# Optimization experiments

Hardware: AMD Instinct MI355X
Metric: run time of the kernel (lower is better)

Reference implementation:

```python
import jax, jax.numpy as jnp
import numpy as np
from jax import lax

DN = ('NCHW', 'OIHW', 'NCHW')

def conv3x3(x, w, b):
    y = lax.conv_general_dilated(x, w, (1, 1), 'SAME', dimension_numbers=DN)
    return y + b[None, :, None, None]

def box_filter(x, ws):
    # depthwise WxW averaging conv, VALID after reflect pad
    C = x.shape[1]
    k = jnp.ones((C, 1, ws, ws), x.dtype) / (ws * ws)
    return lax.conv_general_dilated(x, k, (1, 1), 'VALID', feature_group_count=C,
                                    dimension_numbers=DN)

def compute_std_map(features, ws):
    N, C, H, W = features.shape
    pad = ws // 2
    fp = jnp.pad(features, ((0, 0), (0, 0), (pad, pad), (pad, pad)), mode='reflect')
    local_mean = box_filter(fp, ws)            # [N,C,H,W]
    local_mean_sq = box_filter(fp * fp, ws)
    local_var = jnp.clip(local_mean_sq - local_mean ** 2, 1e-6, None)
    if C == 4:
        cw = jax.nn.softmax(jnp.array([1.0, 1.5, 1.0, 1.5], features.dtype))
    else:
        cw = jax.nn.softmax(jnp.ones((C,), features.dtype))
    result = jnp.sum(jnp.sqrt(local_var) * cw[None, :, None, None], axis=1, keepdims=True)
    return result ** 0.8                        # [N,1,H,W]

def setup_inputs() -> dict:
    key = jax.random.key(0)
    ks = jax.random.split(key, 10)
    inp = {}
    inp['x'] = jax.random.normal(ks[0], (1, 4, 1024, 1024), jnp.float32)
    inp['w1'] = jax.random.normal(ks[1], (32, 4, 3, 3), jnp.float32) * (1.0 / np.sqrt(4 * 9))
    inp['b1'] = jax.random.normal(ks[2], (32,), jnp.float32) * 0.01
    inp['w2'] = jax.random.normal(ks[3], (16, 32, 3, 3), jnp.float32) * (1.0 / np.sqrt(32 * 9))
    inp['b2'] = jax.random.normal(ks[4], (16,), jnp.float32) * 0.01
    inp['w3'] = jax.random.normal(ks[5], (8, 16, 3, 3), jnp.float32) * (1.0 / np.sqrt(16 * 9))
    inp['b3'] = jax.random.normal(ks[6], (8,), jnp.float32) * 0.01
    inp['channel_weights'] = jnp.ones((4,), jnp.float32) / 4.0
    inp['fusion_w'] = jnp.full((1, 3, 1, 1), 1.0 / 3.0, jnp.float32) + \
        jax.random.normal(ks[7], (1, 3, 1, 1), jnp.float32) * 0.02
    inp['fusion_b'] = jnp.zeros((1,), jnp.float32)
    return inp

def reference(x, w1, b1, w2, b2, w3, b3, channel_weights, fusion_w, fusion_b):
    window_sizes = [11, 25, 49]
    # feature extractor
    f = jax.nn.leaky_relu(conv3x3(x, w1, b1), 0.2)
    f = jax.nn.leaky_relu(conv3x3(f, w2, b2), 0.2)
    f = conv3x3(f, w3, b3)                      # [B,8,H,W]
    # multi-scale std maps
    maps = jnp.concatenate([compute_std_map(f, ws) for ws in window_sizes], axis=1)  # [B,3,H,W]
    fused = jax.nn.relu(
        lax.conv_general_dilated(maps, fusion_w, (1, 1), 'VALID', dimension_numbers=DN)
        + fusion_b[None, :, None, None])        # [B,1,H,W]
    # adaptive thresholds
    std_flat = fused.reshape(-1)
    q25 = jnp.quantile(std_flat, 0.25)
    q75 = jnp.quantile(std_flat, 0.75)
    iqr75 = q75 - q25
    global_std = jnp.std(x, axis=(2, 3), keepdims=True, ddof=1)   # [B,4,1,1]
    lower = (q25 - 0.5 * iqr75) * jnp.ones_like(global_std)
    upper = (q75 + 0.5 * iqr75) * jnp.ones_like(global_std)
    gf = jnp.clip(global_std * 5.0, 0.5, 2.0)
    lower = lower * gf
    upper = upper * gf
    cwn = jax.nn.softmax(channel_weights).reshape(1, 4, 1, 1)
    channel_std = jnp.std(x * cwn, axis=(2, 3), keepdims=True, ddof=1)
    cf = jnp.clip(channel_std * 2.0, 0.8, 1.2)
    lower = lower * cf
    upper = upper * cf
    # texture mask
    q30 = jnp.quantile(std_flat, 0.3)
    q70 = jnp.quantile(std_flat, 0.7)
    lower_mean = jnp.mean(lower, axis=1, keepdims=True)           # [B,1,1,1]
    upper_mean = jnp.mean(upper, axis=1, keepdims=True)
    l_t = 0.5 * lower_mean + 0.5 * q30
    u_t = 0.5 * upper_mean + 0.5 * q70
    iqr = q70 - q30
    widen = iqr < 0.01
    l_t = jnp.where(widen, l_t - iqr, l_t)
    u_t = jnp.where(widen, u_t + iqr, u_t)
    diff = u_t - l_t
    mid0 = (l_t + u_t) / 2
    narrow = diff < 0.02
    l_t = jnp.where(narrow, mid0 - 0.01, l_t)
    u_t = jnp.where(narrow, mid0 + 0.01, u_t)
    midpoint = (l_t + u_t) / 2
    scale = u_t - l_t
    normalized = jax.nn.sigmoid(4.0 * (fused - midpoint) / scale)
    nm = jnp.mean(normalized)
    mask = jnp.where(nm > 0.65, 0.1 + 0.5 * normalized,
                     jnp.where(nm < 0.35, 0.2 + 0.5 * normalized,
                               0.15 + 0.55 * normalized))
    return mask
```

## Files before the change

### kernel.cpp

```cpp
#include <hip/hip_runtime.h>
#include <stdint.h>

constexpr int H = 1024, W = 1024;
constexpr int NPIX = H * W;
constexpr int PADM = 24;
constexpr int PROW = W + 2 * PADM;

constexpr size_t OFF_F1H   = 0;
constexpr size_t OFF_F1L   = 67108864;
constexpr size_t OFF_F2H   = 134217728;
constexpr size_t OFF_F2L   = 167772160;
constexpr size_t OFF_F3    = 0;
constexpr size_t OFF_HF    = 33554432;
constexpr size_t OFF_HF2   = 67108864;
constexpr size_t OFF_MAPS  = 100663296;
constexpr size_t OFF_FUSED = OFF_MAPS + 3UL * 4194304;
constexpr size_t OFF_NORM  = OFF_FUSED + 4194304;
constexpr size_t OFF_SMALL = 201326592;
constexpr size_t OFF_STATS  = OFF_SMALL;
constexpr size_t OFF_NMSUM  = OFF_SMALL + 64;
constexpr size_t OFF_HIST   = OFF_SMALL + 128;
constexpr size_t OFF_RSTATE = OFF_HIST + 8192;
constexpr size_t OFF_SCAL   = OFF_RSTATE + 64;
constexpr size_t OFF_WT     = OFF_SCAL + 64;

using short8  = __attribute__((ext_vector_type(8))) short;
using short4v = __attribute__((ext_vector_type(4))) short;
using f32x4   = __attribute__((ext_vector_type(4))) float;

__device__ __forceinline__ int reflect1024(int j) {
    return j < 0 ? -j : (j > 1023 ? 2046 - j : j);
}
__device__ __forceinline__ unsigned short rne_bf16(float v) {
    uint32_t u = __float_as_uint(v);
    return (unsigned short)((u + 0x7FFFu + ((u >> 16) & 1u)) >> 16);
}
__device__ __forceinline__ float bf16f(unsigned short h) {
    return __uint_as_float(((uint32_t)h) << 16);
}

__global__ void wfrag_kernel(const float* __restrict__ w, unsigned short* __restrict__ wfH,
                             unsigned short* __restrict__ wfL, int CIN, int COUT, int NF, int S) {
    int total = NF * S * 512;
    int e = blockIdx.x * 256 + threadIdx.x;
    if (e >= total) return;
    int j = e & 7, l = (e >> 3) & 63;
    int rest = e >> 9;
    int s = rest % S, nf = rest / S;
    int k = s * 32 + ((l >> 4) << 3) + j;
    int n = (l & 15) + 16 * nf;
    float v = 0.f;
    if (k < 9 * CIN && n < COUT) {
        int kk = k / CIN, c = k % CIN;
        int ky = kk / 3, kx = kk - ky * 3;
        v = w[((n * CIN + c) * 3 + ky) * 3 + kx];
    }
    unsigned short h = rne_bf16(v);
    wfH[e] = h;
    wfL[e] = rne_bf16(v - bf16f(h));
}

template <int CIN, int COUT, int S, bool LEAKY, int OUT_MODE, int IN_MODE, int MINW>
__global__ __launch_bounds__(256, MINW) void mconv_kernel(
        const void* __restrict__ inA, const void* __restrict__ inB,
        const unsigned short* __restrict__ wfH, const unsigned short* __restrict__ wfL,
        const float* __restrict__ bias, void* __restrict__ outA, void* __restrict__ outB) {
    constexpr int NF = (COUT + 15) / 16;
    constexpr int RS = 66 * CIN;
    __shared__ __align__(16) unsigned short Ah[6 * RS];
    __shared__ __align__(16) unsigned short Al[6 * RS];

    const int tid = threadIdx.x;
    const int bx = blockIdx.x * 64, by = blockIdx.y * 4;
    const int lane = tid & 63, rw = tid >> 6;

    if constexpr (IN_MODE == 1) {
        constexpr int CROW = RS / 8;
        constexpr int LCP  = (CIN == 32) ? 2 : 1;
        constexpr int TOT  = 12 * CROW;
        constexpr int NLOAD = (TOT + 255) / 256;
        const unsigned short* gh = (const unsigned short*)inA;
        const unsigned short* gl = (const unsigned short*)inB;

        short8 regs[NLOAD];
#pragma unroll
        for (int k = 0; k < NLOAD; ++k) {
            int idx = tid + k * 256;
            short8 v = short8{0, 0, 0, 0, 0, 0, 0, 0};
            if (idx < TOT) {
                int ar = idx / CROW;
                int j  = idx - ar * CROW;
                int r  = ar >> 1;
                int a  = ar & 1;
                int gy = by - 1 + r;
                int gx = bx - 1 + (j >> LCP);
                if ((unsigned)gy < 1024u && (unsigned)gx < 1024u) {
                    const unsigned short* g = (a ? gl : gh) +
                        ((size_t)gy << 10) * CIN + (size_t)(bx - 1) * CIN + (size_t)j * 8;
                    v = *(const short8*)g;
                }
            }
            regs[k] = v;
        }
#pragma unroll
        for (int k = 0; k < NLOAD; ++k) {
            int idx = tid + k * 256;
            if (idx < TOT) {
                int ar = idx / CROW;
                int j  = idx - ar * CROW;
                int r  = ar >> 1;
                int a  = ar & 1;
                unsigned short* dst = (a ? Al : Ah) + r * RS + j * 8;
                *(short8*)dst = regs[k];
            }
        }
    } else {
        constexpr int TOT = 6 * 4 * 66;
        constexpr int NLOAD = (TOT + 255) / 256;
        const float* xin = (const float*)inA;
        float regs[NLOAD];
#pragma unroll
        for (int k = 0; k < NLOAD; ++k) {
            int idx = tid + k * 256;
            float v = 0.f;
            if (idx < TOT) {
                int rc  = idx / 66;
                int px  = idx - rc * 66;
                int r   = rc >> 2, c = rc & 3;
                int gy = by - 1 + r, gx = bx - 1 + px;
                if ((unsigned)gy < 1024u && (unsigned)gx < 1024u)
                    v = xin[(size_t)c * NPIX + ((size_t)gy << 10) + gx];
            }
            regs[k] = v;
        }
#pragma unroll
        for (int k = 0; k < NLOAD; ++k) {
            int idx = tid + k * 256;
            if (idx < TOT) {
                int rc  = idx / 66;
                int px  = idx - rc * 66;
                int r   = rc >> 2, c = rc & 3;
                unsigned short h = rne_bf16(regs[k]);
                Ah[r * RS + px * CIN + c] = h;
                Al[r * RS + px * CIN + c] = rne_bf16(regs[k] - bf16f(h));
            }
        }
    }

    short8 wh[NF][S], wl[NF][S];
#pragma unroll
    for (int nf = 0; nf < NF; ++nf)
#pragma unroll
        for (int s = 0; s < S; ++s) {
            wh[nf][s] = *(const short8*)(wfH + (size_t)((nf * S + s) * 64 + lane) * 8);
            wl[nf][s] = *(const short8*)(wfL + (size_t)((nf * S + s) * 64 + lane) * 8);
        }

    const int nidx = lane & 15;
    f32x4 acc[4][NF];
#pragma unroll
    for (int nf = 0; nf < NF; ++nf) {
        float bv = (nidx + nf * 16 < COUT) ? bias[nidx + nf * 16] : 0.f;
#pragma unroll
        for (int t = 0; t < 4; ++t) acc[t][nf] = f32x4{bv, bv, bv, bv};
    }

    __syncthreads();

    if constexpr (CIN == 32) {
        const int base = rw * RS + (lane & 15) * 32 + (lane >> 4) * 8;
        const unsigned short* pah = Ah + base;
        const unsigned short* pal = Al + base;
#pragma unroll
        for (int s = 0; s < S; ++s) {
            const int ky = s / 3, kx = s - (s / 3) * 3;
#pragma unroll
            for (int t = 0; t < 4; ++t) {
                const int off = ky * RS + kx * 32 + t * 512;
                short8 a = *(const short8*)(pah + off);
                short8 b = *(const short8*)(pal + off);
#pragma unroll
                for (int nf = 0; nf < NF; ++nf) {
                    acc[t][nf] = __builtin_amdgcn_mfma_f32_16x16x32_bf16(a, wh[nf][s], acc[t][nf], 0, 0, 0);
                    acc[t][nf] = __builtin_amdgcn_mfma_f32_16x16x32_bf16(b, wh[nf][s], acc[t][nf], 0, 0, 0);
                    acc[t][nf] = __builtin_amdgcn_mfma_f32_16x16x32_bf16(a, wl[nf][s], acc[t][nf], 0, 0, 0);
                }
            }
        }
    } else if constexpr (CIN == 16) {
        const int g23 = lane >> 5;
        const int base = rw * RS + (lane & 15) * 16 + ((lane >> 4) & 1) * 8;
#pragma unroll
        for (int s = 0; s < S; ++s) {
            const int kk0 = 2 * s, kk1 = 2 * s + 1;
            const int O0 = (kk0 / 3) * RS + (kk0 - (kk0 / 3) * 3) * 16;
            const int O1 = (kk1 <= 8) ? (kk1 / 3) * RS + (kk1 - (kk1 / 3) * 3) * 16 : 0;
            const int offs = base + (g23 ? O1 : O0);
#pragma unroll
            for (int t = 0; t < 4; ++t) {
                short8 a = *(const short8*)(Ah + offs + t * 256);
                short8 b = *(const short8*)(Al + offs + t * 256);
#pragma unroll
                for (int nf = 0; nf < NF; ++nf) {
                    acc[t][nf] = __builtin_amdgcn_mfma_f32_16x16x32_bf16(a, wh[nf][s], acc[t][nf], 0, 0, 0);
                    acc[t][nf] = __builtin_amdgcn_mfma_f32_16x16x32_bf16(b, wh[nf][s], acc[t][nf], 0, 0, 0);
                    acc[t][nf] = __builtin_amdgcn_mfma_f32_16x16x32_bf16(a, wl[nf][s], acc[t][nf], 0, 0, 0);
                }
            }
        }
    } else {
        const int base = rw * RS + (lane & 15) * 4;
        const int g2 = (lane >> 4) * 2;
#pragma unroll
        for (int s = 0; s < S; ++s) {
            int kkA = s * 8 + g2, kkB = kkA + 1;
            int kyA = (kkA * 11) >> 5; int kxA = kkA - kyA * 3;
            int poA = (kkA <= 8) ? kyA * RS + kxA * 4 : 0;
            int kyB = (kkB * 11) >> 5; int kxB = kkB - kyB * 3;
            int poB = (kkB <= 8) ? kyB * RS + kxB * 4 : 0;
#pragma unroll
            for (int t = 0; t < 4; ++t) {
                union { short4v q[2]; short8 o; } ua, ub;
                ua.q[0] = *(const short4v*)(Ah + base + poA + t * 64);
                ua.q[1] = *(const short4v*)(Ah + base + poB + t * 64);
                ub.q[0] = *(const short4v*)(Al + base + poA + t * 64);
                ub.q[1] = *(const short4v*)(Al + base + poB + t * 64);
                short8 a = ua.o, b = ub.o;
#pragma unroll
                for (int nf = 0; nf < NF; ++nf) {
                    acc[t][nf] = __builtin_amdgcn_mfma_f32_16x16x32_bf16(a, wh[nf][s], acc[t][nf], 0, 0, 0);
                    acc[t][nf] = __builtin_amdgcn_mfma_f32_16x16x32_bf16(b, wh[nf][s], acc[t][nf], 0, 0, 0);
                    acc[t][nf] = __builtin_amdgcn_mfma_f32_16x16x32_bf16(a, wl[nf][s], acc[t][nf], 0, 0, 0);
                }
            }
        }
    }

    const int y = by + rw;
    const int mrow = (lane >> 4) * 4;
    if constexpr (OUT_MODE == 0) {
        float* outp = (float*)outA;
        if (nidx < COUT) {
#pragma unroll
            for (int t = 0; t < 4; ++t)
#pragma unroll
                for (int j = 0; j < 4; ++j) {
                    int x = bx + t * 16 + mrow + j;
                    float v = acc[t][0][j];
                    if (LEAKY) v = v >= 0.f ? v : 0.2f * v;
                    outp[(size_t)nidx * NPIX + ((size_t)y << 10) + x] = v;
                }
        }
    } else {
        unsigned short* oh = (unsigned short*)outA;
        unsigned short* ol = (unsigned short*)outB;
#pragma unroll
        for (int t = 0; t < 4; ++t)
#pragma unroll
            for (int nf = 0; nf < NF; ++nf)
#pragma unroll
                for (int j = 0; j < 4; ++j) {
                    float v = acc[t][nf][j];
                    if (LEAKY) v = v >= 0.f ? v : 0.2f * v;
                    int x = bx + t * 16 + mrow + j;
                    size_t off = ((size_t)((y << 10) + x)) * COUT + nf * 16 + nidx;
                    unsigned short hh = rne_bf16(v);
                    oh[off] = hh;
                    ol[off] = rne_bf16(v - bf16f(hh));
                }
    }
}

__global__ void hbox_kernel(const float* __restrict__ f3, float* __restrict__ hf,
                            float* __restrict__ hf2, int p) {
    const int row = blockIdx.x, ch = blockIdx.y, tid = threadIdx.x;
    const float* src = f3 + ch * NPIX + row * W;
    __shared__ float sraw[PROW];
    __shared__ float Pf[PROW + 1], Pf2[PROW + 1];
    __shared__ float wtot[4], wtot2[4];

    for (int i = tid; i < PROW; i += 256)
        sraw[i] = src[reflect1024(i - PADM)];
    __syncthreads();

    float lf[5], lf2[5];
    float sf = 0.f, sf2 = 0.f;
    const int base = tid * 5;
#pragma unroll
    for (int j = 0; j < 5; ++j) {
        int idx = base + j;
        float v = (idx < PROW) ? sraw[idx] : 0.f;
        sf += v;      lf[j] = sf;
        sf2 += v * v; lf2[j] = sf2;
    }
    const int lane = tid & 63, wid = tid >> 6;
    float tf = sf, tf2 = sf2;
#pragma unroll
    for (int off = 1; off < 64; off <<= 1) {
        float a = __shfl_up(tf, off);
        float b = __shfl_up(tf2, off);
        if (lane >= off) { tf += a; tf2 += b; }
    }
    if (lane == 63) { wtot[wid] = tf; wtot2[wid] = tf2; }
    __syncthreads();
    float bse = 0.f, bse2 = 0.f;
    for (int w2 = 0; w2 < wid; ++w2) { bse += wtot[w2]; bse2 += wtot2[w2]; }
    float ex = bse + tf - sf, ex2 = bse2 + tf2 - sf2;
    if (base <= PROW) { Pf[base] = ex; Pf2[base] = ex2; }
#pragma unroll
    for (int j = 0; j < 5; ++j) {
        int idx = base + j + 1;
        if (idx <= PROW) { Pf[idx] = ex + lf[j]; Pf2[idx] = ex2 + lf2[j]; }
    }
    __syncthreads();

    float* df  = hf  + ch * NPIX + row * W;
    float* df2 = hf2 + ch * NPIX + row * W;
    for (int x = tid; x < W; x += 256) {
        int a = x + PADM - p, b = x + PADM + p + 1;
        df[x]  = Pf[b]  - Pf[a];
        df2[x] = Pf2[b] - Pf2[a];
    }
}

constexpr int VRS = 128;
__global__ __launch_bounds__(512) void vbox_kernel(const float* __restrict__ hf,
                                                   const float* __restrict__ hf2,
                                                   float* __restrict__ map,
                                                   int p, float inv_area) {
    const int tid = threadIdx.x;
    const int colIdx = tid & 63, ch = tid >> 6;
    const int col = blockIdx.x * 64 + colIdx;
    const int r0 = blockIdx.y * VRS;
    const float* pf  = hf  + ch * NPIX + col;
    const float* pf2 = hf2 + ch * NPIX + col;

    float S1 = 0.f, S2 = 0.f;
    for (int t = -p; t <= p; ++t) {
        int rr = reflect1024(r0 + t);
        S1 += pf[rr * W];
        S2 += pf2[rr * W];
    }

    __shared__ float ssq[8][8][65];
    const int jj = tid >> 6, cc = tid & 63;
    for (int rb = r0; rb < r0 + VRS; rb += 8) {
#pragma unroll
        for (int j = 0; j < 8; ++j) {
            int r = rb + j;
            float m1 = S1 * inv_area, m2 = S2 * inv_area;
            float var = fmaxf(m2 - m1 * m1, 1e-6f);
            ssq[ch][j][colIdx] = sqrtf(var);
            int radd = reflect1024(r + 1 + p), rsub = reflect1024(r - p);
            S1 += pf[radd * W] - pf[rsub * W];
            S2 += pf2[radd * W] - pf2[rsub * W];
        }
        __syncthreads();
        float a = 0.f;
#pragma unroll
        for (int c8 = 0; c8 < 8; ++c8) a += ssq[c8][jj][cc];
        map[(rb + jj) * W + blockIdx.x * 64 + cc] = powf(a * 0.125f, 0.8f);
        __syncthreads();
    }
}

__global__ void fusion_kernel(const float* __restrict__ maps, const float* __restrict__ fw,
                              const float* __restrict__ fb, float* __restrict__ fused) {
    float w0 = fw[0], w1 = fw[1], w2 = fw[2], b = fb[0];
    for (int i = blockIdx.x * blockDim.x + threadIdx.x; i < NPIX; i += gridDim.x * blockDim.x) {
        float v = maps[i] * w0 + maps[NPIX + i] * w1 + maps[2 * NPIX + i] * w2 + b;
        fused[i] = fmaxf(v, 0.f);
    }
}

__global__ void stats_kernel(const float* __restrict__ x, double* __restrict__ stats) {
    int ch = blockIdx.x >> 6;
    int blk = blockIdx.x & 63;
    const float* p = x + ch * NPIX;
    double s1 = 0.0, s2 = 0.0;
    for (int i = blk * 256 + threadIdx.x; i < NPIX; i += 64 * 256) {
        double v = (double)p[i];
        s1 += v; s2 += v * v;
    }
    __shared__ double b1[256], b2[256];
    b1[threadIdx.x] = s1; b2[threadIdx.x] = s2;
    __syncthreads();
    for (int off = 128; off > 0; off >>= 1) {
        if (threadIdx.x < off) {
            b1[threadIdx.x] += b1[threadIdx.x + off];
            b2[threadIdx.x] += b2[threadIdx.x + off];
        }
        __syncthreads();
    }
    if (threadIdx.x == 0) {
        atomicAdd(&stats[ch * 2 + 0], b1[0]);
        atomicAdd(&stats[ch * 2 + 1], b2[0]);
    }
}

__global__ void init_kernel(double* stats, double* nmsum, uint32_t* hist, uint32_t* rstate) {
    int tid = threadIdx.x;
    for (int i = tid; i < 2048; i += 256) hist[i] = 0u;
    if (tid < 8) stats[tid] = 0.0;
    if (tid == 0) nmsum[0] = 0.0;
    if (tid < 8) rstate[tid] = 0u;
    if (tid < 8) {
        const uint32_t ranks[8] = {262143u, 262144u, 314572u, 314573u,
                                   734002u, 734003u, 786431u, 786432u};
        rstate[8 + tid] = ranks[tid];
    }
}

__global__ void radix_hist_kernel(const float* __restrict__ fused, uint32_t* __restrict__ hist,
                                  const uint32_t* __restrict__ rstate, int pass) {
    __shared__ uint32_t h[8][256];
    int tid = threadIdx.x;
    for (int i = tid; i < 2048; i += 256) ((uint32_t*)h)[i] = 0u;
    __syncthreads();

    uint32_t pref[8];
#pragma unroll
    for (int r = 0; r < 8; ++r) pref[r] = rstate[r];
    uint32_t maskHi = (pass == 0) ? 0u : (0xFFFFFFFFu << (32 - 8 * pass));
    int shift = 24 - 8 * pass;

    for (int i = blockIdx.x * blockDim.x + tid; i < NPIX; i += gridDim.x * blockDim.x) {
        uint32_t u = __float_as_uint(fused[i]);
        uint32_t key = (u & 0x80000000u) ? ~u : (u | 0x80000000u);
        uint32_t bin = (key >> shift) & 0xFFu;
        if (pass == 0) {
            atomicAdd(&h[0][bin], 1u);
        } else {
#pragma unroll
            for (int r = 0; r < 8; ++r) {
                if (((key ^ pref[r]) & maskHi) == 0u)
                    atomicAdd(&h[r][bin], 1u);
            }
        }
    }
    __syncthreads();
    if (pass == 0) {
        for (int i = tid; i < 256; i += 256) {
            uint32_t v = h[0][i];
            if (v)
                for (int r = 0; r < 8; ++r) atomicAdd(&hist[r * 256 + i], v);
        }
    } else {
        for (int i = tid; i < 2048; i += 256) {
            uint32_t v = ((uint32_t*)h)[i];
            if (v) atomicAdd(&hist[i], v);
        }
    }
}

__global__ void radix_scan_kernel(uint32_t* __restrict__ hist, uint32_t* __restrict__ rstate,
                                  int pass) {
    int tid = threadIdx.x;
    int shift = 24 - 8 * pass;
    const int lane = tid & 63, wv = tid >> 6;
    __shared__ uint32_t wsum[4];
    for (int r = 0; r < 8; ++r) {
        uint32_t c = hist[r * 256 + tid];
        uint32_t sc = c;
#pragma unroll
        for (int off = 1; off < 64; off <<= 1) {
            uint32_t t = __shfl_up(sc, off);
            if (lane >= off) sc += t;
        }
        if (lane == 63) wsum[wv] = sc;
        __syncthreads();
        uint32_t base = 0;
        for (int w2 = 0; w2 < wv; ++w2) base += wsum[w2];
        uint32_t incl = base + sc, excl = incl - c;
        uint32_t lr = rstate[8 + r];
        if (lr >= excl && lr < incl) {
            rstate[r] |= ((uint32_t)tid) << shift;
            rstate[8 + r] = lr - excl;
        }
        hist[r * 256 + tid] = 0u;
        __syncthreads();
    }
}

__device__ __forceinline__ float key_to_float(uint32_t k) {
    uint32_t u = (k & 0x80000000u) ? (k & 0x7FFFFFFFu) : ~k;
    return __uint_as_float(u);
}

__global__ void scalar_kernel(const uint32_t* __restrict__ rstate,
                              const double* __restrict__ stats,
                              const float* __restrict__ cw,
                              float* __restrict__ scal) {
    if (threadIdx.x != 0 || blockIdx.x != 0) return;
    float v[8];
#pragma unroll
    for (int r = 0; r < 8; ++r) v[r] = key_to_float(rstate[r]);
    float q25 = v[0] + 0.75f * (v[1] - v[0]);
    float q30 = v[2] + 0.5f * (v[3] - v[2]);
    float q70 = v[4] + 0.5f * (v[5] - v[4]);
    float q75 = v[6] + 0.25f * (v[7] - v[6]);

    const double N = (double)NPIX;
    float gstd[4];
#pragma unroll
    for (int c = 0; c < 4; ++c) {
        double s1 = stats[c * 2 + 0], s2 = stats[c * 2 + 1];
        double var = (s2 - s1 * s1 / N) / (N - 1.0);
        gstd[c] = (float)sqrt(var > 0.0 ? var : 0.0);
    }
    float m = fmaxf(fmaxf(cw[0], cw[1]), fmaxf(cw[2], cw[3]));
    float e0 = expf(cw[0] - m), e1 = expf(cw[1] - m), e2 = expf(cw[2] - m), e3 = expf(cw[3] - m);
    float se = e0 + e1 + e2 + e3;
    float cwn[4] = {e0 / se, e1 / se, e2 / se, e3 / se};

    float iqr75 = q75 - q25;
    float low0 = q25 - 0.5f * iqr75;
    float up0  = q75 + 0.5f * iqr75;
    float lsum = 0.f, usum = 0.f;
#pragma unroll
    for (int c = 0; c < 4; ++c) {
        float gf = fminf(fmaxf(gstd[c] * 5.f, 0.5f), 2.f);
        float cs = cwn[c] * gstd[c];
        float cf = fminf(fmaxf(cs * 2.f, 0.8f), 1.2f);
        lsum += low0 * gf * cf;
        usum += up0 * gf * cf;
    }
    float lmean = 0.25f * lsum, umean = 0.25f * usum;
    float l_t = 0.5f * lmean + 0.5f * q30;
    float u_t = 0.5f * umean + 0.5f * q70;
    float iqr = q70 - q30;
    if (iqr < 0.01f) { l_t -= iqr; u_t += iqr; }
    float diff = u_t - l_t;
    float mid0 = 0.5f * (l_t + u_t);
    if (diff < 0.02f) { l_t = mid0 - 0.01f; u_t = mid0 + 0.01f; }
    scal[0] = 0.5f * (l_t + u_t);
    scal[1] = u_t - l_t;
}

__global__ void sigmoid_kernel(const float* __restrict__ fused, const float* __restrict__ scal,
                               float* __restrict__ normalized, double* __restrict__ nmsum) {
    float mid = scal[0], sc = scal[1];
    float inv = 4.0f / sc;
    float local = 0.f;
    for (int i = blockIdx.x * blockDim.x + threadIdx.x; i < NPIX; i += gridDim.x * blockDim.x) {
        float t = (fused[i] - mid) * inv;
        float n = 1.0f / (1.0f + expf(-t));
        normalized[i] = n;
        local += n;
    }
    __shared__ float red[256];
    red[threadIdx.x] = local;
    __syncthreads();
    for (int off = 128; off > 0; off >>= 1) {
        if (threadIdx.x < off) red[threadIdx.x] += red[threadIdx.x + off];
        __syncthreads();
    }
    if (threadIdx.x == 0) atomicAdd(nmsum, (double)red[0]);
}

__global__ void final_kernel(const float* __restrict__ normalized, const double* __restrict__ nmsum,
                             float* __restrict__ out) {
    float nm = (float)(nmsum[0] / (double)NPIX);
    float a, b;
    if (nm > 0.65f)      { a = 0.10f; b = 0.50f; }
    else if (nm < 0.35f) { a = 0.20f; b = 0.50f; }
    else                 { a = 0.15f; b = 0.55f; }
    for (int i = blockIdx.x * blockDim.x + threadIdx.x; i < NPIX; i += gridDim.x * blockDim.x)
        out[i] = a + b * normalized[i];
}

extern "C" void kernel_launch(void* const* d_in, const int* in_sizes, int n_in,
                              void* d_out, int out_size, void* d_ws, size_t ws_size,
                              hipStream_t stream) {
    const float* x   = (const float*)d_in[0];
    const float* w1  = (const float*)d_in[1];
    const float* b1  = (const float*)d_in[2];
    const float* w2  = (const float*)d_in[3];
    const float* b2  = (const float*)d_in[4];
    const float* w3  = (const float*)d_in[5];
    const float* b3  = (const float*)d_in[6];
    const float* cw  = (const float*)d_in[7];
    const float* fw  = (const float*)d_in[8];
    const float* fb  = (const float*)d_in[9];

    char* ws = (char*)d_ws;
    unsigned short* f1h = (unsigned short*)(ws + OFF_F1H);
    unsigned short* f1l = (unsigned short*)(ws + OFF_F1L);
    unsigned short* f2h = (unsigned short*)(ws + OFF_F2H);
    unsigned short* f2l = (unsigned short*)(ws + OFF_F2L);
    float* f3    = (float*)(ws + OFF_F3);
    float* hf    = (float*)(ws + OFF_HF);
    float* hf2   = (float*)(ws + OFF_HF2);
    float* maps  = (float*)(ws + OFF_MAPS);
    float* fused = (float*)(ws + OFF_FUSED);
    float* norm  = (float*)(ws + OFF_NORM);
    double* stats = (double*)(ws + OFF_STATS);
    double* nmsum = (double*)(ws + OFF_NMSUM);
    uint32_t* hist   = (uint32_t*)(ws + OFF_HIST);
    uint32_t* rstate = (uint32_t*)(ws + OFF_RSTATE);
    float* scal = (float*)(ws + OFF_SCAL);
    unsigned short* wf1H = (unsigned short*)(ws + OFF_WT);
    unsigned short* wf1L = wf1H + 2048;
    unsigned short* wf2H = wf1L + 2048;
    unsigned short* wf2L = wf2H + 4608;
    unsigned short* wf3H = wf2L + 4608;
    unsigned short* wf3L = wf3H + 2560;

    init_kernel<<<1, 256, 0, stream>>>(stats, nmsum, hist, rstate);
    stats_kernel<<<256, 256, 0, stream>>>(x, stats);
    wfrag_kernel<<<(2 * 2 * 512 + 255) / 256, 256, 0, stream>>>(w1, wf1H, wf1L, 4, 32, 2, 2);
    wfrag_kernel<<<(1 * 9 * 512 + 255) / 256, 256, 0, stream>>>(w2, wf2H, wf2L, 32, 16, 1, 9);
    wfrag_kernel<<<(1 * 5 * 512 + 255) / 256, 256, 0, stream>>>(w3, wf3H, wf3L, 16, 8, 1, 5);

    dim3 cgrid(16, 256);
    mconv_kernel<4, 32, 2, true, 1, 0, 4><<<cgrid, 256, 0, stream>>>(
        x, nullptr, wf1H, wf1L, b1, f1h, f1l);
    mconv_kernel<32, 16, 9, true, 1, 1, 3><<<cgrid, 256, 0, stream>>>(
        f1h, f1l, wf2H, wf2L, b2, f2h, f2l);
    mconv_kernel<16, 8, 5, false, 0, 1, 4><<<cgrid, 256, 0, stream>>>(
        f2h, f2l, wf3H, wf3L, b3, f3, nullptr);

    const int wss[3] = {11, 25, 49};
    for (int k = 0; k < 3; ++k) {
        int p = wss[k] / 2;
        float inv_area = 1.0f / (float)(wss[k] * wss[k]);
        hbox_kernel<<<dim3(H, 8), 256, 0, stream>>>(f3, hf, hf2, p);
        vbox_kernel<<<dim3(W / 64, H / VRS), 512, 0, stream>>>(hf, hf2, maps + (size_t)k * NPIX,
                                                               p, inv_area);
    }

    fusion_kernel<<<1024, 256, 0, stream>>>(maps, fw, fb, fused);

    for (int pass = 0; pass < 4; ++pass) {
        radix_hist_kernel<<<256, 256, 0, stream>>>(fused, hist, rstate, pass);
        radix_scan_kernel<<<1, 256, 0, stream>>>(hist, rstate, pass);
    }

    scalar_kernel<<<1, 64, 0, stream>>>(rstate, stats, cw, scal);

    sigmoid_kernel<<<1024, 256, 0, stream>>>(fused, scal, norm, nmsum);
    final_kernel<<<1024, 256, 0, stream>>>(norm, nmsum, (float*)d_out);
}
```

Before: 409.5 us.

## Stage conv output through LDS, shrink vbox rows, recompute sigmoid in final pass

The fp32-output conv path now writes results into shared memory first, then stores them as coalesced rows, so lanes no longer scatter one float per channel. The vertical box filter processes 32 rows per block instead of 128, giving more blocks at the price of more redundant window initialisation per block. The sigmoid pass now only accumulates the mean, and the final pass recomputes the sigmoid from fused, so the normalized buffer is never written or read back. The LDS staging assumes the Ah buffer is large enough and that the tile layout matches COUT*256 elements.

```diff
diff --git a/kernel.cpp b/kernel.cpp
--- a/kernel.cpp
+++ b/kernel.cpp
@@ -15,7 +15,6 @@
 constexpr size_t OFF_HF2   = 67108864;
 constexpr size_t OFF_MAPS  = 100663296;
 constexpr size_t OFF_FUSED = OFF_MAPS + 3UL * 4194304;
-constexpr size_t OFF_NORM  = OFF_FUSED + 4194304;
 constexpr size_t OFF_SMALL = 201326592;
 constexpr size_t OFF_STATS  = OFF_SMALL;
 constexpr size_t OFF_NMSUM  = OFF_SMALL + 64;
@@ -239,17 +238,26 @@
     const int y = by + rw;
     const int mrow = (lane >> 4) * 4;
     if constexpr (OUT_MODE == 0) {
-        float* outp = (float*)outA;
+        __syncthreads();
+        float* smem = (float*)Ah;
         if (nidx < COUT) {
 #pragma unroll
             for (int t = 0; t < 4; ++t)
 #pragma unroll
                 for (int j = 0; j < 4; ++j) {
-                    int x = bx + t * 16 + mrow + j;
                     float v = acc[t][0][j];
                     if (LEAKY) v = v >= 0.f ? v : 0.2f * v;
-                    outp[(size_t)nidx * NPIX + ((size_t)y << 10) + x] = v;
+                    smem[(nidx * 4 + rw) * 66 + t * 16 + mrow + j] = v;
                 }
+        }
+        __syncthreads();
+        float* outp = (float*)outA;
+#pragma unroll
+        for (int k = 0; k < (COUT * 256) / 256; ++k) {
+            int i = tid + k * 256;
+            int px = i & 63, r = (i >> 6) & 3, c = i >> 8;
+            outp[(size_t)c * NPIX + ((size_t)(by + r) << 10) + bx + px] =
+                smem[(c * 4 + r) * 66 + px];
         }
     } else {
         unsigned short* oh = (unsigned short*)outA;
@@ -323,7 +331,7 @@
     }
 }
 
-constexpr int VRS = 128;
+constexpr int VRS = 32;
 __global__ __launch_bounds__(512) void vbox_kernel(const float* __restrict__ hf,
                                                    const float* __restrict__ hf2,
                                                    float* __restrict__ map,
@@ -538,15 +546,13 @@
 }
 
 __global__ void sigmoid_kernel(const float* __restrict__ fused, const float* __restrict__ scal,
-                               float* __restrict__ normalized, double* __restrict__ nmsum) {
+                               double* __restrict__ nmsum) {
     float mid = scal[0], sc = scal[1];
     float inv = 4.0f / sc;
     float local = 0.f;
     for (int i = blockIdx.x * blockDim.x + threadIdx.x; i < NPIX; i += gridDim.x * blockDim.x) {
         float t = (fused[i] - mid) * inv;
-        float n = 1.0f / (1.0f + expf(-t));
-        normalized[i] = n;
-        local += n;
+        local += 1.0f / (1.0f + expf(-t));
     }
     __shared__ float red[256];
     red[threadIdx.x] = local;
@@ -558,15 +564,19 @@
     if (threadIdx.x == 0) atomicAdd(nmsum, (double)red[0]);
 }
 
-__global__ void final_kernel(const float* __restrict__ normalized, const double* __restrict__ nmsum,
-                             float* __restrict__ out) {
+__global__ void final_kernel(const float* __restrict__ fused, const float* __restrict__ scal,
+                             const double* __restrict__ nmsum, float* __restrict__ out) {
     float nm = (float)(nmsum[0] / (double)NPIX);
     float a, b;
     if (nm > 0.65f)      { a = 0.10f; b = 0.50f; }
     else if (nm < 0.35f) { a = 0.20f; b = 0.50f; }
     else                 { a = 0.15f; b = 0.55f; }
-    for (int i = blockIdx.x * blockDim.x + threadIdx.x; i < NPIX; i += gridDim.x * blockDim.x)
-        out[i] = a + b * normalized[i];
+    float mid = scal[0], inv = 4.0f / scal[1];
+    for (int i = blockIdx.x * blockDim.x + threadIdx.x; i < NPIX; i += gridDim.x * blockDim.x) {
+        float t = (fused[i] - mid) * inv;
+        float n = 1.0f / (1.0f + expf(-t));
+        out[i] = a + b * n;
+    }
 }
 
 extern "C" void kernel_launch(void* const* d_in, const int* in_sizes, int n_in,
@@ -593,7 +603,6 @@
     float* hf2   = (float*)(ws + OFF_HF2);
     float* maps  = (float*)(ws + OFF_MAPS);
     float* fused = (float*)(ws + OFF_FUSED);
-    float* norm  = (float*)(ws + OFF_NORM);
     double* stats = (double*)(ws + OFF_STATS);
     double* nmsum = (double*)(ws + OFF_NMSUM);
     uint32_t* hist   = (uint32_t*)(ws + OFF_HIST);
@@ -638,6 +647,6 @@
 
     scalar_kernel<<<1, 64, 0, stream>>>(rstate, stats, cw, scal);
 
-    sigmoid_kernel<<<1024, 256, 0, stream>>>(fused, scal, norm, nmsum);
-    final_kernel<<<1024, 256, 0, stream>>>(norm, nmsum, (float*)d_out);
-}
+    sigmoid_kernel<<<1024, 256, 0, stream>>>(fused, scal, nmsum);
+    final_kernel<<<1024, 256, 0, stream>>>(fused, scal, nmsum, (float*)d_out);
+}
```

Measured after the change: 375.2 us. 1.09x faster.
